# Performance work log

Hardware: AMD Instinct MI355X
Metric: run time of the kernel (lower is better)

## Reference

```python
import jax, jax.numpy as jnp
import numpy as np

H = 121
W = 121
N_INTERP = 200
XRANGE0 = -15.0
YRANGE0 = -15.0
XYSTEP = 0.25
RET_PER_DVA = 280.0  # Curcio linear retinotopy, um per deg
XLOW = XRANGE0 * RET_PER_DVA   # -4200 um
XHIGH = -XLOW
YLOW = YRANGE0 * RET_PER_DVA
YHIGH = -YLOW
STEP_X = (XHIGH - XLOW) / (N_INTERP - 1)
STEP_Y = (YHIGH - YLOW) / (N_INTERP - 1)
OD_OFF_X = 15.5 * RET_PER_DVA  # optic disc location in retinal um
OD_OFF_Y = 1.5 * RET_PER_DVA
AMP_CUTOFF = 0.25
PI = np.pi
TEMP1 = 4.0 * PI  # -2*pi*log(exp(-2)) = 4*pi


def setup_inputs() -> dict:
    key = jax.random.key(0)
    ks = jax.random.split(key, 6)
    B, E = 8, 225
    # stimulus: freq (Hz), amp (xTh), pulse duration (ms)
    freq = jax.random.uniform(ks[0], (B, E)) * 20.0
    amp = jax.random.uniform(ks[1], (B, E)) * 2.0
    pdur = jax.random.uniform(ks[2], (B, E)) * 0.4 + 0.05
    stim = jnp.stack([freq, amp, pdur], axis=-1).astype(jnp.float32)
    # patient params: rho, lam, orient_scale, a0..a4, implant_x/y, rot, loc_od_x/y
    u = jax.random.uniform(ks[3], (B, 13))
    lo = jnp.array([100.0, 0.1, 0.8, 0.5, 0.3, 0.01, 0.5, -0.5, -500.0, -500.0, -0.3, OD_OFF_X - 100.0, OD_OFF_Y - 100.0])
    hi = jnp.array([400.0, 0.9, 1.2, 1.5, 0.7, 0.10, 1.5, 0.5, 500.0, 500.0, 0.3, OD_OFF_X + 100.0, OD_OFF_Y + 100.0])
    params = (lo + u * (hi - lo)).astype(jnp.float32)
    # 15x15 electrode grid, 300 um pitch, centered
    coords = (jnp.arange(15, dtype=jnp.float32) - 7.0) * 300.0
    gx, gy = jnp.meshgrid(coords, coords)
    elec_x = gx.reshape(1, -1)
    elec_y = gy.reshape(1, -1)
    # precomputed axon bundle tangent slopes on n_interp x n_interp grid, [y, x]
    slopes = jax.random.uniform(ks[4], (N_INTERP, N_INTERP), minval=-PI / 2, maxval=PI / 2).astype(jnp.float32)
    # pixelgrid exactly as in source: swapaxes(indices(shape),0,2).reshape(-1,2)
    pixelgrid = jnp.asarray(np.swapaxes(np.indices((H, W)), 0, 2).reshape(-1, 2), dtype=jnp.float32)
    return dict(stim=stim, params=params, elec_x=elec_x, elec_y=elec_y, slopes=slopes, pixelgrid=pixelgrid)


def _interp_bilinear(grid, qx, qy):
    # grid: [Ny, Nx] indexed [y, x]; matches tfa interpolate_bilinear(indexing='xy')
    ny, nx = grid.shape
    fx = jnp.clip(jnp.floor(qx), 0.0, nx - 2)
    fy = jnp.clip(jnp.floor(qy), 0.0, ny - 2)
    ix = fx.astype(jnp.int32)
    iy = fy.astype(jnp.int32)
    ax = jnp.clip(qx - fx, 0.0, 1.0)
    ay = jnp.clip(qy - fy, 0.0, 1.0)
    g00 = grid[iy, ix]
    g01 = grid[iy, ix + 1]
    g10 = grid[iy + 1, ix]
    g11 = grid[iy + 1, ix + 1]
    top = g00 + ax * (g01 - g00)
    bot = g10 + ax * (g11 - g10)
    return top + ay * (bot - top)


def reference(stim, params, elec_x, elec_y, slopes, pixelgrid):
    freq, amp, pdur = stim[..., 0], stim[..., 1], stim[..., 2]  # [B, E]
    rho = params[:, 0:1]
    lam = params[:, 1:2]
    orient_scale = params[:, 2:3]
    a0, a1, a2, a3, a4 = (params[:, i:i + 1] for i in range(3, 8))
    implant_x = params[:, 8:9]
    implant_y = params[:, 9:10]
    rot = params[:, 10:11]
    loc_od_x = params[:, 11:12]
    # rotate + translate electrodes (retinal um), [B, E]
    cr, sr = jnp.cos(rot), jnp.sin(rot)
    ex = elec_x * cr - elec_y * sr + implant_x
    ey = elec_x * sr + elec_y * cr + implant_y
    offx = loc_od_x - OD_OFF_X
    # bilinear interp of axon tangents at shifted electrode positions
    qx = (ex - offx - XLOW) / STEP_X
    qy = (ey - YLOW) / STEP_Y
    thetas = _interp_bilinear(slopes, qx, qy)
    thetas = jnp.where(thetas < -PI / 2, thetas + PI, thetas) * orient_scale
    # per electrode-phosphene MVG params
    rho_scaled = jnp.maximum(rho * amp * a3, 1.0)
    lam_scaled = jnp.clip(lam * 0.45 ** (-a4) * pdur ** a4, 0.0, 0.99)
    bright = jnp.where(amp > AMP_CUTOFF, a0 * jnp.maximum(amp, 1e-5) ** a1 + a2 * freq, 0.0)
    temp2 = jnp.sqrt(1.0 - lam_scaled ** 2)
    sy = rho_scaled / (TEMP1 * temp2)
    sx = rho_scaled * temp2 / TEMP1
    s, c = jnp.sin(thetas), jnp.cos(thetas)
    # cov = R diag(sx, sy) R^T, expanded analytically (symmetric 2x2)
    cov00 = sx * c * c + sy * s * s
    cov01 = (sx - sy) * s * c
    cov11 = sx * s * s + sy * c * c
    det = cov00 * cov11 - cov01 * cov01
    inv00 = cov11 / det
    inv01 = -cov01 / det
    inv11 = cov00 / det
    # electrode centers in pixel coords
    center_x = (ex / RET_PER_DVA - XRANGE0) / XYSTEP
    center_y = H - (ey / RET_PER_DVA - YRANGE0) / XYSTEP
    # quadratic form over all pixels: [P, B, E]
    d0 = pixelgrid[:, None, None, 0] - center_x[None]
    d1 = pixelgrid[:, None, None, 1] - center_y[None]
    t3 = d0 * d0 * inv00[None] + 2.0 * d0 * d1 * inv01[None] + d1 * d1 * inv11[None]
    imgs = jnp.sum(jnp.exp(-0.5 * t3) * bright[None], axis=-1)  # [P, B]
    img = imgs.T.reshape(-1, H, W)  # matches tf transpose+reshape
    return jnp.flip(img, axis=1)    # tf.image.flip_up_down
```

## Files before the change

kernel.cpp:

```cpp
#include <hip/hip_runtime.h>
#include <math.h>

#define Hh 121
#define Ww 121
#define NPI 200
#define Bb 8
#define Ee 225
#define NPIX (Hh * Ww)
#define TS 16
#define XT 8
#define YT 8

#define RPD      280.0f
#define XLOWc   (-4200.0f)
#define STEPc   (8400.0f / 199.0f)
#define ODXc     4340.0f
#define PIc      3.14159265358979323846f
#define TEMP1c  (4.0f * PIc)
#define NHL     (-0.72134752044448170368f)
#define CULL_T   20.0f
#define NL2_045  1.15200309344504995f

#if __has_builtin(__builtin_amdgcn_exp2f)
#define EXP2F(x) __builtin_amdgcn_exp2f(x)
#else
#define EXP2F(x) exp2f(x)
#endif
#if __has_builtin(__builtin_amdgcn_logf)
#define LOG2F(x) __builtin_amdgcn_logf(x)
#else
#define LOG2F(x) log2f(x)
#endif

#define MAXC 232

extern "C" __global__ void __launch_bounds__(256)
mvg_fused(const float* __restrict__ stim, const float* __restrict__ params,
          const float* __restrict__ elec_x, const float* __restrict__ elec_y,
          const float* __restrict__ slopes, float* __restrict__ out)
{
    __shared__ __align__(16) float4 scA[MAXC];
    __shared__ __align__(8)  float2 scB[MAXC];
    __shared__ int scnt;

    const int b   = blockIdx.z;
    const int txb = blockIdx.x;
    const int tyb = blockIdx.y;
    const int tid = threadIdx.x;

    if (tid == 0) scnt = 0;
    __syncthreads();

    const int   jmin = txb * TS;
    const int   jmax = min(jmin + TS - 1, Ww - 1);
    const int   imin = tyb * TS;
    const int   imax = min(imin + TS - 1, Hh - 1);
    const float pxminf = (float)jmin, pxmaxf = (float)jmax;
    const float pyminf = (float)(Hh - 1 - imax), pymaxf = (float)(Hh - 1 - imin);

    if (tid < Ee) {
        const float* p = params + b * 13;
        const float rho = p[0], lam = p[1], osc = p[2];
        const float pa0 = p[3], pa1 = p[4], pa2 = p[5], pa3 = p[6], pa4 = p[7];
        const float impx = p[8], impy = p[9], rot = p[10], locx = p[11];

        const float cr = cosf(rot), sr = sinf(rot);
        const float exl = elec_x[tid], eyl = elec_y[tid];
        const float exv = exl * cr - eyl * sr + impx;
        const float eyv = exl * sr + eyl * cr + impy;

        const float offx = locx - ODXc;
        const float qx = (exv - offx - XLOWc) / STEPc;
        const float qy = (eyv - XLOWc) / STEPc;
        const float fx = fminf(fmaxf(floorf(qx), 0.0f), (float)(NPI - 2));
        const float fy = fminf(fmaxf(floorf(qy), 0.0f), (float)(NPI - 2));
        const int ix = (int)fx, iy = (int)fy;
        const float ax = fminf(fmaxf(qx - fx, 0.0f), 1.0f);
        const float ay = fminf(fmaxf(qy - fy, 0.0f), 1.0f);
        const float g00 = slopes[iy * NPI + ix];
        const float g01 = slopes[iy * NPI + ix + 1];
        const float g10 = slopes[(iy + 1) * NPI + ix];
        const float g11 = slopes[(iy + 1) * NPI + ix + 1];
        const float top = g00 + ax * (g01 - g00);
        const float bot = g10 + ax * (g11 - g10);
        float th = top + ay * (bot - top);
        th = (th < -0.5f * PIc) ? th + PIc : th;
        th *= osc;

        const float* st = stim + (b * Ee + tid) * 3;
        const float freq = st[0], amp = st[1], pdur = st[2];

        const float rho_s = fmaxf(rho * amp * pa3, 1.0f);
        float lam_s = lam * EXP2F(pa4 * (LOG2F(pdur) + NL2_045));
        lam_s = fminf(fmaxf(lam_s, 0.0f), 0.99f);
        const float bright =
            (amp > 0.25f)
                ? (pa0 * EXP2F(pa1 * LOG2F(fmaxf(amp, 1e-5f))) + pa2 * freq)
                : 0.0f;

        const float temp2 = sqrtf(1.0f - lam_s * lam_s);
        const float sy_ = rho_s / (TEMP1c * temp2);
        const float sx_ = rho_s * temp2 / TEMP1c;
        const float s = sinf(th), c = cosf(th);
        const float cov00 = sx_ * c * c + sy_ * s * s;
        const float cov01 = (sx_ - sy_) * s * c;
        const float cov11 = sx_ * s * s + sy_ * c * c;
        const float det = cov00 * cov11 - cov01 * cov01;
        const float i00 = cov11 / det;
        const float i01 = -cov01 / det;
        const float i11 = cov00 / det;

        const float cx = (exv / RPD + 15.0f) * 4.0f;
        const float cy = (float)Hh - (eyv / RPD + 15.0f) * 4.0f;

        const float A = i00 * NHL;
        const float B = i01 * 2.0f * NHL;
        const float C = i11 * NHL;

        const float a = -A, bq = -B, cc = -C;
        const float lam_min = 0.5f * ((a + cc) - sqrtf((a - cc) * (a - cc) + bq * bq));
        float R;
        if (bright != 0.0f && lam_min > 0.0f)      R = sqrtf(CULL_T / lam_min) + 0.5f;
        else if (bright != 0.0f)                   R = 1e9f;
        else                                       R = -1e9f;

        const bool live = (cx + R >= pxminf) && (cx - R <= pxmaxf) &&
                          (cy + R >= pyminf) && (cy - R <= pymaxf);
        if (live) {
            const int pos = atomicAdd(&scnt, 1);
            scA[pos] = make_float4(cx, cy, A, B);
            scB[pos] = make_float2(C, bright);
        }
    }
    __syncthreads();

    const int cnt = scnt;
    if (tid < 4) {
        scA[cnt + tid] = make_float4(0.0f, 0.0f, 0.0f, 0.0f);
        scB[cnt + tid] = make_float2(0.0f, 0.0f);
    }
    __syncthreads();
    const int n = (cnt + 3) & ~3;

    const int lx = tid & (TS - 1);
    const int ly = tid >> 4;
    const int j  = jmin + lx;
    const int i  = imin + ly;
    const float px = (float)j;
    const float py = (float)(Hh - 1 - i);

    float ac0 = 0.0f, ac1 = 0.0f, ac2 = 0.0f, ac3 = 0.0f;

#define BODY(k, acc) {                                          \
        const float4 v = scA[e + (k)];                          \
        const float2 w = scB[e + (k)];                          \
        const float dx = px - v.x;                              \
        const float dy = py - v.y;                              \
        const float u  = fmaf(dx, v.z, dy * v.w);               \
        const float t  = fmaf(dy * dy, w.x, dx * u);            \
        acc = fmaf(w.y, EXP2F(t), acc);                         \
    }

    #pragma unroll 1
    for (int e = 0; e < n; e += 4) {
        BODY(0, ac0)
        BODY(1, ac1)
        BODY(2, ac2)
        BODY(3, ac3)
    }
#undef BODY

    if (i < Hh && j < Ww)
        out[b * NPIX + i * Ww + j] = (ac0 + ac1) + (ac2 + ac3);
}

extern "C" void kernel_launch(void* const* d_in, const int* in_sizes, int n_in,
                              void* d_out, int out_size, void* d_ws, size_t ws_size,
                              hipStream_t stream) {
    const float* stim   = (const float*)d_in[0];
    const float* params = (const float*)d_in[1];
    const float* ex     = (const float*)d_in[2];
    const float* ey     = (const float*)d_in[3];
    const float* slopes = (const float*)d_in[4];
    float* out = (float*)d_out;

    dim3 grid(XT, YT, Bb);
    mvg_fused<<<grid, 256, 0, stream>>>(stim, params, ex, ey, slopes, out);
}
```

Before: 73.98 us.

## Split into prep and render kernels with per-tile culled electrode lists

Splits the fused kernel in two. A prep kernel computes each electrode's Gaussian parameters once per batch per 8-tile group, and writes per-tile culled record lists to workspace using wave ballot compaction. Before, every one of the 64 tiles recomputed all 225 electrodes. A render kernel then loads its tile's list into shared memory and accumulates the exponentials. The prep math also swaps divisions and sin/cos for hardware rcp and sin intrinsics. The cost is a second launch and a global-memory round trip, and record order is now nondeterministic.

```diff
diff --git a/kernel.cpp b/kernel.cpp
--- a/kernel.cpp
+++ b/kernel.cpp
@@ -10,13 +10,16 @@
 #define TS 16
 #define XT 8
 #define YT 8
+#define NTILE (XT * YT)
+#define SLOTS 228
 
 #define RPD      280.0f
 #define XLOWc   (-4200.0f)
-#define STEPc   (8400.0f / 199.0f)
+#define RSTEP   (199.0f / 8400.0f)
 #define ODXc     4340.0f
 #define PIc      3.14159265358979323846f
-#define TEMP1c  (4.0f * PIc)
+#define INV2PI   0.15915494309189535f
+#define INV4PI   0.07957747154594767f
 #define NHL     (-0.72134752044448170368f)
 #define CULL_T   20.0f
 #define NL2_045  1.15200309344504995f
@@ -31,47 +34,53 @@
 #else
 #define LOG2F(x) log2f(x)
 #endif
-
-#define MAXC 232
+#if __has_builtin(__builtin_amdgcn_sinf)
+#define SINR(x) __builtin_amdgcn_sinf((x) * INV2PI)
+#define COSR(x) __builtin_amdgcn_cosf((x) * INV2PI)
+#else
+#define SINR(x) sinf(x)
+#define COSR(x) cosf(x)
+#endif
+#if __has_builtin(__builtin_amdgcn_rcpf)
+#define RCPF(x) __builtin_amdgcn_rcpf(x)
+#else
+#define RCPF(x) (1.0f / (x))
+#endif
+
 
 extern "C" __global__ void __launch_bounds__(256)
-mvg_fused(const float* __restrict__ stim, const float* __restrict__ params,
-          const float* __restrict__ elec_x, const float* __restrict__ elec_y,
-          const float* __restrict__ slopes, float* __restrict__ out)
+mvg_prep(const float* __restrict__ stim, const float* __restrict__ params,
+         const float* __restrict__ elec_x, const float* __restrict__ elec_y,
+         const float* __restrict__ slopes, int* __restrict__ counts,
+         float4* __restrict__ recs)
 {
-    __shared__ __align__(16) float4 scA[MAXC];
-    __shared__ __align__(8)  float2 scB[MAXC];
-    __shared__ int scnt;
-
-    const int b   = blockIdx.z;
-    const int txb = blockIdx.x;
-    const int tyb = blockIdx.y;
-    const int tid = threadIdx.x;
-
-    if (tid == 0) scnt = 0;
+    const int b    = blockIdx.y;
+    const int tg   = blockIdx.x;
+    const int tid  = threadIdx.x;
+    const int lane = tid & 63;
+    const int wv   = tid >> 6;
+
+    __shared__ int scnt8[8];
+    __shared__ int wbase[4];
+    if (tid < 8) scnt8[tid] = 0;
     __syncthreads();
 
-    const int   jmin = txb * TS;
-    const int   jmax = min(jmin + TS - 1, Ww - 1);
-    const int   imin = tyb * TS;
-    const int   imax = min(imin + TS - 1, Hh - 1);
-    const float pxminf = (float)jmin, pxmaxf = (float)jmax;
-    const float pyminf = (float)(Hh - 1 - imax), pymaxf = (float)(Hh - 1 - imin);
-
-    if (tid < Ee) {
+    float cx = 0.f, cy = 0.f, A = 0.f, B = 0.f, C = 0.f, R = -1e9f, bright = 0.f;
+    const bool has = tid < Ee;
+    if (has) {
         const float* p = params + b * 13;
         const float rho = p[0], lam = p[1], osc = p[2];
         const float pa0 = p[3], pa1 = p[4], pa2 = p[5], pa3 = p[6], pa4 = p[7];
         const float impx = p[8], impy = p[9], rot = p[10], locx = p[11];
 
-        const float cr = cosf(rot), sr = sinf(rot);
+        const float cr = COSR(rot), sr = SINR(rot);
         const float exl = elec_x[tid], eyl = elec_y[tid];
         const float exv = exl * cr - eyl * sr + impx;
         const float eyv = exl * sr + eyl * cr + impy;
 
         const float offx = locx - ODXc;
-        const float qx = (exv - offx - XLOWc) / STEPc;
-        const float qy = (eyv - XLOWc) / STEPc;
+        const float qx = (exv - offx - XLOWc) * RSTEP;
+        const float qy = (eyv - XLOWc) * RSTEP;
         const float fx = fminf(fmaxf(floorf(qx), 0.0f), (float)(NPI - 2));
         const float fy = fminf(fmaxf(floorf(qy), 0.0f), (float)(NPI - 2));
         const int ix = (int)fx, iy = (int)fy;
@@ -93,76 +102,113 @@
         const float rho_s = fmaxf(rho * amp * pa3, 1.0f);
         float lam_s = lam * EXP2F(pa4 * (LOG2F(pdur) + NL2_045));
         lam_s = fminf(fmaxf(lam_s, 0.0f), 0.99f);
-        const float bright =
-            (amp > 0.25f)
-                ? (pa0 * EXP2F(pa1 * LOG2F(fmaxf(amp, 1e-5f))) + pa2 * freq)
-                : 0.0f;
+        bright = (amp > 0.25f)
+                   ? (pa0 * EXP2F(pa1 * LOG2F(fmaxf(amp, 1e-5f))) + pa2 * freq)
+                   : 0.0f;
 
         const float temp2 = sqrtf(1.0f - lam_s * lam_s);
-        const float sy_ = rho_s / (TEMP1c * temp2);
-        const float sx_ = rho_s * temp2 / TEMP1c;
-        const float s = sinf(th), c = cosf(th);
+        const float rt2  = RCPF(temp2);
+        const float sy_ = rho_s * INV4PI * rt2;
+        const float sx_ = rho_s * temp2 * INV4PI;
+        const float s = SINR(th), c = COSR(th);
         const float cov00 = sx_ * c * c + sy_ * s * s;
         const float cov01 = (sx_ - sy_) * s * c;
         const float cov11 = sx_ * s * s + sy_ * c * c;
-        const float det = cov00 * cov11 - cov01 * cov01;
-        const float i00 = cov11 / det;
-        const float i01 = -cov01 / det;
-        const float i11 = cov00 / det;
-
-        const float cx = (exv / RPD + 15.0f) * 4.0f;
-        const float cy = (float)Hh - (eyv / RPD + 15.0f) * 4.0f;
-
-        const float A = i00 * NHL;
-        const float B = i01 * 2.0f * NHL;
-        const float C = i11 * NHL;
+        const float det  = cov00 * cov11 - cov01 * cov01;
+        const float rdet = RCPF(det);
+        const float i00 =  cov11 * rdet;
+        const float i01 = -cov01 * rdet;
+        const float i11 =  cov00 * rdet;
+
+        cx = exv * (1.0f / 70.0f) + 60.0f;
+        cy = 61.0f - eyv * (1.0f / 70.0f);
+
+        A = i00 * NHL;
+        B = i01 * 2.0f * NHL;
+        C = i11 * NHL;
 
         const float a = -A, bq = -B, cc = -C;
         const float lam_min = 0.5f * ((a + cc) - sqrtf((a - cc) * (a - cc) + bq * bq));
-        float R;
         if (bright != 0.0f && lam_min > 0.0f)      R = sqrtf(CULL_T / lam_min) + 0.5f;
         else if (bright != 0.0f)                   R = 1e9f;
         else                                       R = -1e9f;
-
-        const bool live = (cx + R >= pxminf) && (cx - R <= pxmaxf) &&
-                          (cy + R >= pyminf) && (cy - R <= pymaxf);
+    }
+
+    for (int t = 0; t < 8; ++t) {
+        const int tile = tg * 8 + t;
+        const int tx = tile & (XT - 1), ty = tile >> 3;
+        const float pxmin = (float)(tx * TS);
+        const float pxmax = (float)min(tx * TS + TS - 1, Ww - 1);
+        const float pymax = (float)(Hh - 1 - ty * TS);
+        const float pymin = (float)(Hh - 1 - min(ty * TS + TS - 1, Hh - 1));
+
+        const bool live = has &&
+            (cx + R >= pxmin) && (cx - R <= pxmax) &&
+            (cy + R >= pymin) && (cy - R <= pymax);
+
+        const unsigned long long m = __ballot(live);
+        const int pre = (int)__popcll(m & ((1ull << lane) - 1ull));
+        if (lane == 0) wbase[wv] = atomicAdd(&scnt8[t], (int)__popcll(m));
+        const int base = wbase[wv];
         if (live) {
-            const int pos = atomicAdd(&scnt, 1);
-            scA[pos] = make_float4(cx, cy, A, B);
-            scB[pos] = make_float2(C, bright);
+            float4* dst = recs + ((size_t)(b * NTILE + tile) * SLOTS + base + pre) * 2;
+            dst[0] = make_float4(cx, cy, A, B);
+            dst[1] = make_float4(C, bright, 0.0f, 0.0f);
         }
     }
     __syncthreads();
 
-    const int cnt = scnt;
-    if (tid < 4) {
-        scA[cnt + tid] = make_float4(0.0f, 0.0f, 0.0f, 0.0f);
-        scB[cnt + tid] = make_float2(0.0f, 0.0f);
-    }
+    for (int t = 0; t < 8; ++t) {
+        const int tile = tg * 8 + t;
+        const int n  = scnt8[t];
+        const int nr = (n + 3) & ~3;
+        if (tid < nr - n) {
+            float4* dst = recs + ((size_t)(b * NTILE + tile) * SLOTS + n + tid) * 2;
+            dst[0] = make_float4(0.f, 0.f, 0.f, 0.f);
+            dst[1] = make_float4(0.f, 0.f, 0.f, 0.f);
+        }
+        if (tid == 0) counts[b * NTILE + tile] = n;
+    }
+}
+
+extern "C" __global__ void __launch_bounds__(256)
+mvg_render(const int* __restrict__ counts, const float4* __restrict__ recs,
+           float* __restrict__ out)
+{
+    __shared__ __align__(16) float4 sL[SLOTS * 2];
+
+    const int b    = blockIdx.z;
+    const int tile = blockIdx.y * XT + blockIdx.x;
+    const int tid  = threadIdx.x;
+
+    const int n  = counts[b * NTILE + tile];
+    const int nr = (n + 3) & ~3;
+
+    const float4* g = recs + (size_t)(b * NTILE + tile) * SLOTS * 2;
+    for (int u = tid; u < nr * 2; u += 256) sL[u] = g[u];
     __syncthreads();
-    const int n = (cnt + 3) & ~3;
 
     const int lx = tid & (TS - 1);
     const int ly = tid >> 4;
-    const int j  = jmin + lx;
-    const int i  = imin + ly;
+    const int j  = blockIdx.x * TS + lx;
+    const int i  = blockIdx.y * TS + ly;
     const float px = (float)j;
     const float py = (float)(Hh - 1 - i);
 
-    float ac0 = 0.0f, ac1 = 0.0f, ac2 = 0.0f, ac3 = 0.0f;
+    float ac0 = 0.f, ac1 = 0.f, ac2 = 0.f, ac3 = 0.f;
 
 #define BODY(k, acc) {                                          \
-        const float4 v = scA[e + (k)];                          \
-        const float2 w = scB[e + (k)];                          \
+        const float4 v = sL[2 * (e + (k))];                     \
+        const float4 w = sL[2 * (e + (k)) + 1];                 \
         const float dx = px - v.x;                              \
         const float dy = py - v.y;                              \
-        const float u  = fmaf(dx, v.z, dy * v.w);               \
-        const float t  = fmaf(dy * dy, w.x, dx * u);            \
-        acc = fmaf(w.y, EXP2F(t), acc);                         \
+        const float u_ = fmaf(dx, v.z, dy * v.w);               \
+        const float t_ = fmaf(dy * dy, w.x, dx * u_);           \
+        acc = fmaf(w.y, EXP2F(t_), acc);                        \
     }
 
     #pragma unroll 1
-    for (int e = 0; e < n; e += 4) {
+    for (int e = 0; e < nr; e += 4) {
         BODY(0, ac0)
         BODY(1, ac1)
         BODY(2, ac2)
@@ -184,6 +230,12 @@
     const float* slopes = (const float*)d_in[4];
     float* out = (float*)d_out;
 
-    dim3 grid(XT, YT, Bb);
-    mvg_fused<<<grid, 256, 0, stream>>>(stim, params, ex, ey, slopes, out);
+    int*    counts = (int*)d_ws;
+    float4* recs   = (float4*)((char*)d_ws + 4096);
+
+    dim3 gridA(XT, Bb);
+    mvg_prep<<<gridA, 256, 0, stream>>>(stim, params, ex, ey, slopes, counts, recs);
+
+    dim3 gridB(XT, YT, Bb);
+    mvg_render<<<gridB, 256, 0, stream>>>(counts, recs, out);
 }
```

New measurement: 77.41 us. 4.6% more time.
